# Kernel tuning notes

Hardware: AMD Instinct MI355X
Metric: run time of the kernel (lower is better)

## Reference

```python
import jax, jax.numpy as jnp
import numpy as np

EPS = 1e-5

def _rmsnorm(x, g):
    xf = x.astype(jnp.float32)
    rms = jnp.sqrt(jnp.mean(xf * xf + EPS, axis=-1, keepdims=True))
    return (xf / rms * g).astype(x.dtype)

def setup_inputs() -> dict:
    key = jax.random.key(0)
    ks = jax.random.split(key, 10)
    B, S, D, H, F = 2, 2048, 1024, 16, 4096
    s = 0.02
    return {
        "x": jax.random.normal(ks[0], (B, S, D), jnp.float32),
        "g1": jnp.ones((D,), jnp.float32),
        "wq": jax.random.normal(ks[1], (D, D), jnp.float32) * s,
        "wk": jax.random.normal(ks[2], (D, D), jnp.float32) * s,
        "wv": jax.random.normal(ks[3], (D, D), jnp.float32) * s,
        "wo": jax.random.normal(ks[4], (D, D), jnp.float32) * s,
        "g2": jnp.ones((D,), jnp.float32),
        "w1": jax.random.normal(ks[5], (F, D), jnp.float32) * s,
        "w2": jax.random.normal(ks[6], (D, F), jnp.float32) * s,
        "w3": jax.random.normal(ks[7], (F, D), jnp.float32) * s,
    }

def reference(x, g1, wq, wk, wv, wo, g2, w1, w2, w3):
    B, S, D = x.shape
    H = 16
    hd = D // H
    # --- attention sublayer ---
    xn = _rmsnorm(x, g1)
    q = jnp.einsum('bsd,ed->bse', xn, wq).reshape(B, S, H, hd).transpose(0, 2, 1, 3)
    k = jnp.einsum('bsd,ed->bse', xn, wk).reshape(B, S, H, hd).transpose(0, 2, 1, 3)
    v = jnp.einsum('bsd,ed->bse', xn, wv).reshape(B, S, H, hd).transpose(0, 2, 1, 3)
    scores = jnp.einsum('bhqd,bhkd->bhqk', q, k) / jnp.sqrt(jnp.float32(hd))
    mask = jnp.tril(jnp.ones((S, S), bool))  # causal
    neg = jnp.finfo(scores.dtype).min
    scores = jnp.where(mask[None, None], scores, neg)
    probs = jax.nn.softmax(scores, axis=-1)
    o = jnp.einsum('bhqk,bhkd->bhqd', probs, v)
    o = o.transpose(0, 2, 1, 3).reshape(B, S, D)
    attn_out = jnp.einsum('bsv,dv->bsd', o, wo)
    h = x + attn_out
    # --- SwiGLU sublayer ---
    hn = _rmsnorm(h, g2)
    p1 = jnp.einsum('fd,bsd->bsf', w1, hn)
    p3 = jnp.einsum('fd,bsd->bsf', w3, hn)
    ffn = jnp.einsum('df,bsf->bsd', w2, jax.nn.silu(p1) * p3)
    return h + ffn
```

## Files before the change

kernel.cpp:

```cpp
#include <hip/hip_runtime.h>

typedef __attribute__((ext_vector_type(8))) short short8;
typedef __attribute__((ext_vector_type(4))) float f32x4;

__device__ __forceinline__ unsigned short f2b(float f) {
  union { float f; unsigned u; } v; v.f = f;
  unsigned r = v.u + 0x7fffu + ((v.u >> 16) & 1u);
  return (unsigned short)(r >> 16);
}
__device__ __forceinline__ float b2f(unsigned short b) {
  union { unsigned u; float f; } v; v.u = ((unsigned)b) << 16; return v.f;
}

__device__ __forceinline__ void gload_lds16(const void* g, void* l) {
  __builtin_amdgcn_global_load_lds(
      (const __attribute__((address_space(1))) void*)g,
      (__attribute__((address_space(3))) void*)l, 16, 0, 0);
}

__global__ __launch_bounds__(256) void cvt_k(const float* __restrict__ s,
                                             unsigned short* __restrict__ d, int n4) {
  int i = blockIdx.x * 256 + threadIdx.x;
  if (i >= n4) return;
  float4 v = ((const float4*)s)[i];
  ushort4 o;
  o.x = f2b(v.x); o.y = f2b(v.y); o.z = f2b(v.z); o.w = f2b(v.w);
  ((ushort4*)d)[i] = o;
}

__global__ __launch_bounds__(256) void rmsnorm_k(const float* __restrict__ x,
                                                 const float* __restrict__ g,
                                                 unsigned short* __restrict__ out) {
  const int row = blockIdx.x, tid = threadIdx.x;
  const float4 v = ((const float4*)(x + (size_t)row * 1024))[tid];
  float ss = v.x*v.x + v.y*v.y + v.z*v.z + v.w*v.w;
  #pragma unroll
  for (int d = 32; d > 0; d >>= 1) ss += __shfl_down(ss, d);
  __shared__ float red[4];
  if ((tid & 63) == 0) red[tid >> 6] = ss;
  __syncthreads();
  const float tot = red[0] + red[1] + red[2] + red[3];
  const float sc = rsqrtf(tot * (1.0f/1024.0f) + 1e-5f);
  const float4 gg = ((const float4*)g)[tid];
  ushort4 o;
  o.x = f2b(v.x * sc * gg.x); o.y = f2b(v.y * sc * gg.y);
  o.z = f2b(v.z * sc * gg.z); o.w = f2b(v.w * sc * gg.w);
  ((ushort4*)(out + (size_t)row * 1024))[tid] = o;
}

__global__ __launch_bounds__(256) void gate_k(unsigned short* __restrict__ p13) {
  const size_t i = (size_t)blockIdx.x * 256 + threadIdx.x;
  const int r = (int)(i >> 9);
  const int fc = ((int)i & 511) * 8;
  unsigned short* p1 = p13 + (size_t)r * 8192 + fc;
  const unsigned short* p3 = p13 + (size_t)r * 8192 + 4096 + fc;
  ushort4 a0 = ((const ushort4*)p1)[0], a1 = ((const ushort4*)p1)[1];
  ushort4 b0 = ((const ushort4*)p3)[0], b1 = ((const ushort4*)p3)[1];
  unsigned short va[8] = {a0.x,a0.y,a0.z,a0.w,a1.x,a1.y,a1.z,a1.w};
  unsigned short vb[8] = {b0.x,b0.y,b0.z,b0.w,b1.x,b1.y,b1.z,b1.w};
  unsigned short vo[8];
  #pragma unroll
  for (int j = 0; j < 8; ++j) {
    float f1 = b2f(va[j]), f3 = b2f(vb[j]);
    float s = f1 / (1.0f + __expf(-f1));
    vo[j] = f2b(s * f3);
  }
  ushort4 o0 = {vo[0],vo[1],vo[2],vo[3]}, o1 = {vo[4],vo[5],vo[6],vo[7]};
  ((ushort4*)p1)[0] = o0; ((ushort4*)p1)[1] = o1;
}

template<int EPI>
__global__ __launch_bounds__(256) void gemm_bt(
    const unsigned short* __restrict__ A, const unsigned short* __restrict__ W,
    int N, int K, int lda,
    unsigned short* __restrict__ Cb, const float* __restrict__ res,
    float* __restrict__ Cf, int ldc)
{
  __shared__ unsigned short sA[4096];
  __shared__ unsigned short sB[4096];
  const int tid = threadIdx.x;
  const int w = tid >> 6, l = tid & 63;
  const int l15 = l & 15, l4 = l >> 4;
  const int bm = blockIdx.y * 128, bn = blockIdx.x * 128;
  const int wm = (w >> 1) * 64, wn = (w & 1) * 64;
  const int c0 = w * 128 + l;
  const int ra0 = c0 >> 2,        ka0 = (c0 & 3) * 8;
  const int ra1 = (c0 + 64) >> 2, ka1 = ((c0 + 64) & 3) * 8;
  const unsigned short* Ar0 = A + (size_t)(bm + ra0) * lda + ka0;
  const unsigned short* Ar1 = A + (size_t)(bm + ra1) * lda + ka1;
  const unsigned short* Wr0 = W + (size_t)(bn + ra0) * K + ka0;
  const unsigned short* Wr1 = W + (size_t)(bn + ra1) * K + ka1;
  f32x4 acc[4][4];
  const f32x4 z4 = {0.f, 0.f, 0.f, 0.f};
  #pragma unroll
  for (int i = 0; i < 4; ++i)
    #pragma unroll
    for (int j = 0; j < 4; ++j) acc[i][j] = z4;

  for (int kt = 0; kt < K; kt += 32) {
    gload_lds16(Ar0 + kt, &sA[w * 1024]);
    gload_lds16(Ar1 + kt, &sA[w * 1024 + 512]);
    gload_lds16(Wr0 + kt, &sB[w * 1024]);
    gload_lds16(Wr1 + kt, &sB[w * 1024 + 512]);
    __syncthreads();
    short8 af[4], bf[4];
    #pragma unroll
    for (int mi = 0; mi < 4; ++mi)
      af[mi] = *(const short8*)&sA[(wm + mi*16 + l15)*32 + l4*8];
    #pragma unroll
    for (int ni = 0; ni < 4; ++ni)
      bf[ni] = *(const short8*)&sB[(wn + ni*16 + l15)*32 + l4*8];
    #pragma unroll
    for (int mi = 0; mi < 4; ++mi)
      #pragma unroll
      for (int ni = 0; ni < 4; ++ni)
        acc[mi][ni] = __builtin_amdgcn_mfma_f32_16x16x32_bf16(af[mi], bf[ni], acc[mi][ni], 0, 0, 0);
    __syncthreads();
  }
  #pragma unroll
  for (int mi = 0; mi < 4; ++mi)
    #pragma unroll
    for (int ni = 0; ni < 4; ++ni) {
      const int row0 = bm + wm + mi*16 + l4*4;
      const int col  = bn + wn + ni*16 + l15;
      #pragma unroll
      for (int r = 0; r < 4; ++r) {
        const float v = acc[mi][ni][r];
        if (EPI == 0) {
          Cb[(size_t)(row0 + r) * ldc + col] = f2b(v);
        } else {
          const size_t o = (size_t)(row0 + r) * ldc + col;
          Cf[o] = res[o] + v;
        }
      }
    }
}

__global__ __launch_bounds__(512, 2) void gemm256_bt(
    const unsigned short* __restrict__ A, const unsigned short* __restrict__ W,
    int K, int lda, unsigned short* __restrict__ Cb, int ldc, int nbx)
{
  __shared__ unsigned short sA[4][8192];
  __shared__ unsigned short sB[4][8192];
  const int tid = threadIdx.x;
  const int w = tid >> 6, l = tid & 63;
  const int l15 = l & 15, l4 = l >> 4;
  const int nwg = nbx * gridDim.y;
  const int flat = blockIdx.y * nbx + blockIdx.x;
  const int q8 = nwg >> 3;
  const int sw = (flat & 7) * q8 + (flat >> 3);
  const int bm = (sw / nbx) * 256, bn = (sw % nbx) * 256;

  int rowl[2], coll[2];
  #pragma unroll
  for (int i = 0; i < 2; ++i) {
    const int g = w * 128 + i * 64 + l;
    const int s = g >> 6, j = g & 63;
    const int r = j >> 2, c8 = (j & 3) * 8;
    rowl[i] = s * 16 + r;
    coll[i] = c8 ^ ((r & 8) << 1);
  }
  const unsigned short* As0 = A + (size_t)(bm + rowl[0]) * lda + coll[0];
  const unsigned short* As1 = A + (size_t)(bm + rowl[1]) * lda + coll[1];
  const unsigned short* Ws0 = W + (size_t)(bn + rowl[0]) * K + coll[0];
  const unsigned short* Ws1 = W + (size_t)(bn + rowl[1]) * K + coll[1];
  const int d0 = w * 1024, d1 = w * 1024 + 512;

  const int swzr = (l4 * 8) ^ ((l15 & 8) << 1);
  const int aoff = (w >> 2) * 4096 + l15 * 32 + swzr;
  const int boff = (w & 3) * 2048 + l15 * 32 + swzr;

  f32x4 acc[8][4];
  const f32x4 z4 = {0.f, 0.f, 0.f, 0.f};
  #pragma unroll
  for (int i = 0; i < 8; ++i)
    #pragma unroll
    for (int j = 0; j < 4; ++j) acc[i][j] = z4;

  const int NT = K >> 5;
  #pragma unroll
  for (int p = 0; p < 3; ++p) {
    const int ko = p * 32;
    gload_lds16(As0 + ko, &sA[p][d0]);
    gload_lds16(As1 + ko, &sA[p][d1]);
    gload_lds16(Ws0 + ko, &sB[p][d0]);
    gload_lds16(Ws1 + ko, &sB[p][d1]);
  }
  asm volatile("s_waitcnt vmcnt(8)" ::: "memory");
  __builtin_amdgcn_s_barrier();

  for (int t = 0; t < NT; ++t) {
    const unsigned short* a_ = sA[t & 3];
    const unsigned short* b_ = sB[t & 3];
    const bool st = (t + 3 < NT);
    const int nb = (t + 3) & 3;
    const int ko = (t + 3) * 32;
    short8 bfr[4], afr[4];
    #pragma unroll
    for (int ni = 0; ni < 4; ++ni) bfr[ni] = *(const short8*)&b_[boff + ni * 512];
    #pragma unroll
    for (int mi = 0; mi < 4; ++mi) afr[mi] = *(const short8*)&a_[aoff + mi * 512];
    if (st) { gload_lds16(As0 + ko, &sA[nb][d0]); gload_lds16(Ws0 + ko, &sB[nb][d0]); }
    __builtin_amdgcn_s_barrier();
    asm volatile("s_waitcnt lgkmcnt(0)" ::: "memory");
    __builtin_amdgcn_sched_barrier(0);
    __builtin_amdgcn_s_setprio(1);
    #pragma unroll
    for (int mi = 0; mi < 4; ++mi)
      #pragma unroll
      for (int ni = 0; ni < 4; ++ni)
        acc[mi][ni] = __builtin_amdgcn_mfma_f32_16x16x32_bf16(bfr[ni], afr[mi], acc[mi][ni], 0, 0, 0);
    __builtin_amdgcn_s_setprio(0);
    __builtin_amdgcn_s_barrier();
    #pragma unroll
    for (int mi = 0; mi < 4; ++mi) afr[mi] = *(const short8*)&a_[aoff + (mi + 4) * 512];
    if (st) { gload_lds16(As1 + ko, &sA[nb][d1]); gload_lds16(Ws1 + ko, &sB[nb][d1]); }
    __builtin_amdgcn_s_barrier();
    asm volatile("s_waitcnt lgkmcnt(0)" ::: "memory");
    __builtin_amdgcn_sched_barrier(0);
    __builtin_amdgcn_s_setprio(1);
    #pragma unroll
    for (int mi = 0; mi < 4; ++mi)
      #pragma unroll
      for (int ni = 0; ni < 4; ++ni)
        acc[mi + 4][ni] = __builtin_amdgcn_mfma_f32_16x16x32_bf16(bfr[ni], afr[mi], acc[mi + 4][ni], 0, 0, 0);
    __builtin_amdgcn_s_setprio(0);
    if (t < NT - 3)       asm volatile("s_waitcnt vmcnt(8)" ::: "memory");
    else if (t == NT - 3) asm volatile("s_waitcnt vmcnt(4)" ::: "memory");
    else                  asm volatile("s_waitcnt vmcnt(0)" ::: "memory");
    __builtin_amdgcn_s_barrier();
  }
  #pragma unroll
  for (int mi = 0; mi < 8; ++mi) {
    const int row = bm + (w >> 2) * 128 + mi * 16 + l15;
    #pragma unroll
    for (int ni = 0; ni < 4; ++ni) {
      const int col = bn + (w & 3) * 64 + ni * 16 + l4 * 4;
      ushort4 o = { f2b(acc[mi][ni][0]), f2b(acc[mi][ni][1]),
                    f2b(acc[mi][ni][2]), f2b(acc[mi][ni][3]) };
      *(ushort4*)&Cb[(size_t)row * ldc + col] = o;
    }
  }
}

__global__ __launch_bounds__(256) void vtrans_k(const unsigned short* __restrict__ QKV,
                                                unsigned short* __restrict__ VT) {
  __shared__ unsigned short sT[4096];
  const int st = blockIdx.x, dt = blockIdx.y, b = blockIdx.z;
  const int tid = threadIdx.x;
  #pragma unroll
  for (int half = 0; half < 2; ++half) {
    const int c = tid + half * 256;
    const int r = c >> 3;
    const int ch = c & 7;
    const unsigned short* src =
        QKV + (size_t)(b*2048 + st*64 + r) * 3072 + 2048 + dt*64 + ch*8;
    short8 v = *(const short8*)src;
    *(short8*)&sT[r*64 + ((ch ^ ((r >> 3) & 7)) * 8)] = v;
  }
  __syncthreads();
  #pragma unroll
  for (int half = 0; half < 2; ++half) {
    const int c = tid + half * 256;
    const int od = c >> 3;
    const int oc = c & 7;
    unsigned short tmp[8];
    #pragma unroll
    for (int j = 0; j < 8; ++j) {
      const int srow = oc*8 + j;
      const int chunk = (od >> 3) ^ ((srow >> 3) & 7);
      tmp[j] = sT[srow*64 + chunk*8 + (od & 7)];
    }
    *(short8*)&VT[(size_t)(b*1024 + dt*64 + od) * 2048 + st*64 + oc*8] = *(short8*)tmp;
  }
}

__global__ __launch_bounds__(256) void attn_k(const unsigned short* __restrict__ QKV,
                                              const unsigned short* __restrict__ VT,
                                              unsigned short* __restrict__ Ob)
{
  const int LDQ = 3072;
  const float C2 = 0.125f * 1.44269504088896f;
  const int b = blockIdx.y >> 4, h = blockIdx.y & 15;
  const int tid = threadIdx.x;
  const int w = tid >> 6, l = tid & 63;
  const int l15 = l & 15, l4 = l >> 4;
  const unsigned short* Qg  = QKV + (size_t)(b * 2048) * LDQ + h * 64;
  const unsigned short* Kg  = Qg + 1024;
  const unsigned short* VTg = VT + (size_t)(b * 1024 + h * 64) * 2048;

  __shared__ unsigned short sK[2][4096];
  __shared__ unsigned short sVT[2][4096];
  __shared__ unsigned short sP[4][1152];

  const int rc0 = tid >> 3;
  const int ch0 = (tid & 7) ^ (rc0 & 7);
  const int rc1 = rc0 + 32;
  const unsigned short* Ks0 = Kg  + (size_t)rc0 * LDQ  + ch0 * 8;
  const unsigned short* Ks1 = Kg  + (size_t)rc1 * LDQ  + ch0 * 8;
  const unsigned short* Vs0 = VTg + (size_t)rc0 * 2048 + ch0 * 8;
  const unsigned short* Vs1 = VTg + (size_t)rc1 * 2048 + ch0 * 8;
  const int wun0 = w * 512;
  const int wun1 = 2048 + w * 512;
  const f32x4 z4 = {0.f,0.f,0.f,0.f};

#define ASTAGE(buf, t) do { \
    const size_t ko = (size_t)(t) * 64 * LDQ; const int vo = (t) * 64; \
    gload_lds16(Ks0 + ko, &sK[buf][wun0]); \
    gload_lds16(Ks1 + ko, &sK[buf][wun1]); \
    gload_lds16(Vs0 + vo, &sVT[buf][wun0]); \
    gload_lds16(Vs1 + vo, &sVT[buf][wun1]); } while (0)

  #pragma unroll
  for (int qp = 0; qp < 2; ++qp) {
    const int qtile = (qp == 0) ? (31 - (int)blockIdx.x) : (int)blockIdx.x;
    const int qb = qtile * 64;
    const int qw = qb + w * 16;
    short8 qf[2];
    #pragma unroll
    for (int hc = 0; hc < 2; ++hc)
      qf[hc] = *(const short8*)&Qg[(size_t)(qw + l15) * LDQ + hc*32 + l4*8];

    f32x4 accO[4];
    #pragma unroll
    for (int dt = 0; dt < 4; ++dt) accO[dt] = z4;
    float m_run = -1e30f, l_run = 0.f;

    const int ntB = qtile + 1;
    ASTAGE(0, 0);
    __syncthreads();
    int cur = 0;
    for (int t = 0; t < ntB; ++t) {
      if (t + 1 < ntB) ASTAGE(cur ^ 1, t + 1);
      const int kv = t * 64;
      const unsigned short* Kb = sK[cur];
      const unsigned short* Vb = sVT[cur];
      const int lim = qw + 15 - kv;
      f32x4 sAcc[4];
      #pragma unroll
      for (int nt = 0; nt < 4; ++nt) sAcc[nt] = z4;
      __builtin_amdgcn_s_setprio(1);
      #pragma unroll
      for (int nt = 0; nt < 4; ++nt) {
        if (nt * 16 <= lim) {
          const int krow = nt*16 + l15;
          const short8 kf0 = *(const short8*)&Kb[krow*64 + ((l4 ^ (krow & 7)) * 8)];
          const short8 kf1 = *(const short8*)&Kb[krow*64 + (((4 + l4) ^ (krow & 7)) * 8)];
          sAcc[nt] = __builtin_amdgcn_mfma_f32_16x16x32_bf16(kf0, qf[0], sAcc[nt], 0,0,0);
          sAcc[nt] = __builtin_amdgcn_mfma_f32_16x16x32_bf16(kf1, qf[1], sAcc[nt], 0,0,0);
        }
      }
      __builtin_amdgcn_s_setprio(0);
      const bool bound = (kv + 63 > qw);
      float p[16];
      float mx = -1e30f;
      #pragma unroll
      for (int nt = 0; nt < 4; ++nt)
        #pragma unroll
        for (int r = 0; r < 4; ++r) {
          float s = (nt * 16 <= lim) ? sAcc[nt][r] * C2 : -1e30f;
          if (bound && (kv + nt*16 + l4*4 + r > qw + l15)) s = -1e30f;
          p[nt*4 + r] = s;
          mx = fmaxf(mx, s);
        }
      mx = fmaxf(mx, __shfl_xor(mx, 16));
      mx = fmaxf(mx, __shfl_xor(mx, 32));
      const bool resc = mx > m_run + 8.0f;
      const float mn = resc ? mx : m_run;
      const float f = resc ? exp2f(m_run - mn) : 1.0f;
      m_run = mn;
      float rs = 0.f;
      #pragma unroll
      for (int j = 0; j < 16; ++j) { p[j] = exp2f(p[j] - mn); rs += p[j]; }
      rs += __shfl_xor(rs, 16);
      rs += __shfl_xor(rs, 32);
      l_run = l_run * f + rs;
      if (__any(resc)) {
        float fr[4];
        #pragma unroll
        for (int r = 0; r < 4; ++r) fr[r] = __shfl(f, (l & 48) + l4*4 + r);
        #pragma unroll
        for (int dt = 0; dt < 4; ++dt)
          #pragma unroll
          for (int r = 0; r < 4; ++r) accO[dt][r] *= fr[r];
      }
      #pragma unroll
      for (int nt = 0; nt < 4; ++nt) {
        ushort4 pk = { f2b(p[nt*4]), f2b(p[nt*4+1]), f2b(p[nt*4+2]), f2b(p[nt*4+3]) };
        *(ushort4*)&sP[w][l15*72 + nt*16 + l4*4] = pk;
      }
      short8 pf[2];
      #pragma unroll
      for (int kc = 0; kc < 2; ++kc)
        pf[kc] = *(const short8*)&sP[w][l15*72 + kc*32 + l4*8];
      __builtin_amdgcn_s_setprio(1);
      #pragma unroll
      for (int dt = 0; dt < 4; ++dt) {
        const int vrow = dt*16 + l15;
        const short8 vf0 = *(const short8*)&Vb[vrow*64 + ((l4 ^ (vrow & 7)) * 8)];
        const short8 vf1 = *(const short8*)&Vb[vrow*64 + (((4 + l4) ^ (vrow & 7)) * 8)];
        accO[dt] = __builtin_amdgcn_mfma_f32_16x16x32_bf16(pf[0], vf0, accO[dt], 0,0,0);
        accO[dt] = __builtin_amdgcn_mfma_f32_16x16x32_bf16(pf[1], vf1, accO[dt], 0,0,0);
      }
      __builtin_amdgcn_s_setprio(0);
      __syncthreads();
      cur ^= 1;
    }
    float lr[4];
    #pragma unroll
    for (int r = 0; r < 4; ++r) lr[r] = __shfl(l_run, (l & 48) + l4*4 + r);
    #pragma unroll
    for (int dt = 0; dt < 4; ++dt)
      #pragma unroll
      for (int r = 0; r < 4; ++r) {
        const int row = qw + l4*4 + r;
        Ob[(size_t)(b*2048 + row) * 1024 + h*64 + dt*16 + l15] = f2b(accO[dt][r] / lr[r]);
      }
  }
#undef ASTAGE
}

extern "C" void kernel_launch(void* const* d_in, const int* in_sizes, int n_in,
                              void* d_out, int out_size, void* d_ws, size_t ws_size,
                              hipStream_t stream) {
  const float* x  = (const float*)d_in[0];
  const float* g1 = (const float*)d_in[1];
  const float* wq = (const float*)d_in[2];
  const float* wk = (const float*)d_in[3];
  const float* wv = (const float*)d_in[4];
  const float* wo = (const float*)d_in[5];
  const float* g2 = (const float*)d_in[6];
  const float* w1 = (const float*)d_in[7];
  const float* w2 = (const float*)d_in[8];
  const float* w3 = (const float*)d_in[9];
  float* out = (float*)d_out;
  char* ws = (char*)d_ws;
  (void)in_sizes; (void)n_in; (void)out_size; (void)ws_size;

  unsigned short* Wqkv = (unsigned short*)(ws + 0);
  unsigned short* Wo   = (unsigned short*)(ws + 6291456);
  unsigned short* W13  = (unsigned short*)(ws + 8388608);
  unsigned short* W2   = (unsigned short*)(ws + 25165824);
  unsigned short* XN   = (unsigned short*)(ws + 33554432);
  unsigned short* QKV  = (unsigned short*)(ws + 41943040);
  unsigned short* OB   = (unsigned short*)(ws + 67108864);
  unsigned short* VTb  = (unsigned short*)(ws + 75497472);
  unsigned short* P13  = (unsigned short*)(ws + 41943040);
  float*          H    = (float*)(ws + 109051904);

  cvt_k<<<1024, 256, 0, stream>>>(wq, Wqkv,             262144);
  cvt_k<<<1024, 256, 0, stream>>>(wk, Wqkv + 1048576,   262144);
  cvt_k<<<1024, 256, 0, stream>>>(wv, Wqkv + 2097152,   262144);
  cvt_k<<<1024, 256, 0, stream>>>(wo, Wo,               262144);
  cvt_k<<<4096, 256, 0, stream>>>(w1, W13,             1048576);
  cvt_k<<<4096, 256, 0, stream>>>(w3, W13 + 4194304,   1048576);
  cvt_k<<<4096, 256, 0, stream>>>(w2, W2,              1048576);

  rmsnorm_k<<<4096, 256, 0, stream>>>(x, g1, XN);
  gemm256_bt<<<dim3(12, 16), 512, 0, stream>>>(XN, Wqkv, 1024, 1024, QKV, 3072, 12);
  vtrans_k<<<dim3(32, 16, 2), 256, 0, stream>>>(QKV, VTb);
  attn_k<<<dim3(16, 32), 256, 0, stream>>>(QKV, VTb, OB);
  gemm_bt<1><<<dim3(8, 32), 256, 0, stream>>>(OB, Wo, 1024, 1024, 1024,
                                              nullptr, x, H, 1024);
  rmsnorm_k<<<4096, 256, 0, stream>>>(H, g2, XN);
  gemm256_bt<<<dim3(32, 16), 512, 0, stream>>>(XN, W13, 1024, 1024, P13, 8192, 32);
  gate_k<<<8192, 256, 0, stream>>>(P13);
  gemm_bt<1><<<dim3(8, 32), 256, 0, stream>>>(P13, W2, 1024, 4096, 8192,
                                              nullptr, H, out, 1024);
}
```

Measured before the change: 496.8 us.

## Pipeline 128x128 GEMM with 4-stage LDS ring, swizzle, and vectorized epilogue

Replaces the single-buffered 128-tile GEMM with a 4-buffer LDS ring that prefetches three K-tiles ahead using explicit vmcnt waits and a single barrier per iteration. It also adds an XOR swizzle against LDS bank conflicts, grouped workgroup ordering for L2 reuse, and swapped MFMA operands so the epilogue can write contiguous vectorized bf16/float4 stores. The QKV projection moves from the 256-tile kernel to this 128-tile kernel to get more workgroups. The costs are higher LDS use per block and the risk that the hand-written waitcnt schedule is fragile.

```diff
diff --git a/kernel.cpp b/kernel.cpp
--- a/kernel.cpp
+++ b/kernel.cpp
@@ -70,26 +70,42 @@
 }
 
 template<int EPI>
-__global__ __launch_bounds__(256) void gemm_bt(
+__global__ __launch_bounds__(256, 2) void gemm128p(
     const unsigned short* __restrict__ A, const unsigned short* __restrict__ W,
-    int N, int K, int lda,
-    unsigned short* __restrict__ Cb, const float* __restrict__ res,
-    float* __restrict__ Cf, int ldc)
+    int K, int lda, unsigned short* __restrict__ Cb, const float* __restrict__ res,
+    float* __restrict__ Cf, int ldc, int nbx)
 {
-  __shared__ unsigned short sA[4096];
-  __shared__ unsigned short sB[4096];
+  __shared__ unsigned short sA[4][4096];
+  __shared__ unsigned short sB[4][4096];
   const int tid = threadIdx.x;
   const int w = tid >> 6, l = tid & 63;
   const int l15 = l & 15, l4 = l >> 4;
-  const int bm = blockIdx.y * 128, bn = blockIdx.x * 128;
+  const int nwg = nbx * gridDim.y;
+  const int flat = blockIdx.y * nbx + blockIdx.x;
+  const int q8 = nwg >> 3;
+  const int sw = (flat & 7) * q8 + (flat >> 3);
+  const int bm = (sw / nbx) * 128, bn = (sw % nbx) * 128;
   const int wm = (w >> 1) * 64, wn = (w & 1) * 64;
-  const int c0 = w * 128 + l;
-  const int ra0 = c0 >> 2,        ka0 = (c0 & 3) * 8;
-  const int ra1 = (c0 + 64) >> 2, ka1 = ((c0 + 64) & 3) * 8;
-  const unsigned short* Ar0 = A + (size_t)(bm + ra0) * lda + ka0;
-  const unsigned short* Ar1 = A + (size_t)(bm + ra1) * lda + ka1;
-  const unsigned short* Wr0 = W + (size_t)(bn + ra0) * K + ka0;
-  const unsigned short* Wr1 = W + (size_t)(bn + ra1) * K + ka1;
+
+  int rowl[2], coll[2];
+  #pragma unroll
+  for (int i = 0; i < 2; ++i) {
+    const int g = i * 256 + w * 64 + l;
+    const int s = g >> 6, j = g & 63;
+    const int r = j >> 2, c8 = (j & 3) * 8;
+    rowl[i] = s * 16 + r;
+    coll[i] = c8 ^ ((r & 8) << 1);
+  }
+  const unsigned short* As0 = A + (size_t)(bm + rowl[0]) * lda + coll[0];
+  const unsigned short* As1 = A + (size_t)(bm + rowl[1]) * lda + coll[1];
+  const unsigned short* Ws0 = W + (size_t)(bn + rowl[0]) * K + coll[0];
+  const unsigned short* Ws1 = W + (size_t)(bn + rowl[1]) * K + coll[1];
+  const int d0 = w * 512, d1 = 2048 + w * 512;
+
+  const int swzr = (l4 * 8) ^ ((l15 & 8) << 1);
+  const int aoff = (w >> 1) * 2048 + l15 * 32 + swzr;
+  const int boff = (w & 1) * 2048 + l15 * 32 + swzr;
+
   f32x4 acc[4][4];
   const f32x4 z4 = {0.f, 0.f, 0.f, 0.f};
   #pragma unroll
@@ -97,43 +113,67 @@
     #pragma unroll
     for (int j = 0; j < 4; ++j) acc[i][j] = z4;
 
-  for (int kt = 0; kt < K; kt += 32) {
-    gload_lds16(Ar0 + kt, &sA[w * 1024]);
-    gload_lds16(Ar1 + kt, &sA[w * 1024 + 512]);
-    gload_lds16(Wr0 + kt, &sB[w * 1024]);
-    gload_lds16(Wr1 + kt, &sB[w * 1024 + 512]);
-    __syncthreads();
-    short8 af[4], bf[4];
+  const int NT = K >> 5;
+  #pragma unroll
+  for (int p = 0; p < 3; ++p) {
+    const size_t ko = (size_t)p * 32;
+    gload_lds16(As0 + ko, &sA[p][d0]);
+    gload_lds16(As1 + ko, &sA[p][d1]);
+    gload_lds16(Ws0 + ko, &sB[p][d0]);
+    gload_lds16(Ws1 + ko, &sB[p][d1]);
+  }
+  asm volatile("s_waitcnt vmcnt(8)" ::: "memory");
+  __builtin_amdgcn_s_barrier();
+
+  for (int t = 0; t < NT; ++t) {
+    const unsigned short* a_ = sA[t & 3];
+    const unsigned short* b_ = sB[t & 3];
+    if (t + 3 < NT) {
+      const int nb = (t + 3) & 3;
+      const size_t ko = (size_t)(t + 3) * 32;
+      gload_lds16(As0 + ko, &sA[nb][d0]);
+      gload_lds16(As1 + ko, &sA[nb][d1]);
+      gload_lds16(Ws0 + ko, &sB[nb][d0]);
+      gload_lds16(Ws1 + ko, &sB[nb][d1]);
+    }
+    short8 afr[4], bfr[4];
+    #pragma unroll
+    for (int ni = 0; ni < 4; ++ni) bfr[ni] = *(const short8*)&b_[boff + ni * 512];
+    #pragma unroll
+    for (int mi = 0; mi < 4; ++mi) afr[mi] = *(const short8*)&a_[aoff + mi * 512];
+    asm volatile("s_waitcnt lgkmcnt(0)" ::: "memory");
+    __builtin_amdgcn_sched_barrier(0);
+    __builtin_amdgcn_s_setprio(1);
     #pragma unroll
     for (int mi = 0; mi < 4; ++mi)
-      af[mi] = *(const short8*)&sA[(wm + mi*16 + l15)*32 + l4*8];
-    #pragma unroll
-    for (int ni = 0; ni < 4; ++ni)
-      bf[ni] = *(const short8*)&sB[(wn + ni*16 + l15)*32 + l4*8];
-    #pragma unroll
-    for (int mi = 0; mi < 4; ++mi)
       #pragma unroll
       for (int ni = 0; ni < 4; ++ni)
-        acc[mi][ni] = __builtin_amdgcn_mfma_f32_16x16x32_bf16(af[mi], bf[ni], acc[mi][ni], 0, 0, 0);
-    __syncthreads();
-  }
-  #pragma unroll
-  for (int mi = 0; mi < 4; ++mi)
+        acc[mi][ni] = __builtin_amdgcn_mfma_f32_16x16x32_bf16(bfr[ni], afr[mi], acc[mi][ni], 0, 0, 0);
+    __builtin_amdgcn_s_setprio(0);
+    if (t < NT - 3)       asm volatile("s_waitcnt vmcnt(8)" ::: "memory");
+    else if (t == NT - 3) asm volatile("s_waitcnt vmcnt(4)" ::: "memory");
+    else                  asm volatile("s_waitcnt vmcnt(0)" ::: "memory");
+    __builtin_amdgcn_s_barrier();
+  }
+  #pragma unroll
+  for (int mi = 0; mi < 4; ++mi) {
+    const int row = bm + wm + mi * 16 + l15;
     #pragma unroll
     for (int ni = 0; ni < 4; ++ni) {
-      const int row0 = bm + wm + mi*16 + l4*4;
-      const int col  = bn + wn + ni*16 + l15;
-      #pragma unroll
-      for (int r = 0; r < 4; ++r) {
-        const float v = acc[mi][ni][r];
-        if (EPI == 0) {
-          Cb[(size_t)(row0 + r) * ldc + col] = f2b(v);
-        } else {
-          const size_t o = (size_t)(row0 + r) * ldc + col;
-          Cf[o] = res[o] + v;
-        }
+      const int col = bn + wn + ni * 16 + l4 * 4;
+      if (EPI == 0) {
+        ushort4 o = { f2b(acc[mi][ni][0]), f2b(acc[mi][ni][1]),
+                      f2b(acc[mi][ni][2]), f2b(acc[mi][ni][3]) };
+        *(ushort4*)&Cb[(size_t)row * ldc + col] = o;
+      } else {
+        const size_t o = (size_t)row * ldc + col;
+        const float4 rv = *(const float4*)&res[o];
+        float4 ov = { rv.x + acc[mi][ni][0], rv.y + acc[mi][ni][1],
+                      rv.z + acc[mi][ni][2], rv.w + acc[mi][ni][3] };
+        *(float4*)&Cf[o] = ov;
       }
     }
+  }
 }
 
 __global__ __launch_bounds__(512, 2) void gemm256_bt(
@@ -457,14 +497,15 @@
   cvt_k<<<4096, 256, 0, stream>>>(w2, W2,              1048576);
 
   rmsnorm_k<<<4096, 256, 0, stream>>>(x, g1, XN);
-  gemm256_bt<<<dim3(12, 16), 512, 0, stream>>>(XN, Wqkv, 1024, 1024, QKV, 3072, 12);
+  gemm128p<0><<<dim3(24, 32), 256, 0, stream>>>(XN, Wqkv, 1024, 1024,
+                                                QKV, nullptr, nullptr, 3072, 24);
   vtrans_k<<<dim3(32, 16, 2), 256, 0, stream>>>(QKV, VTb);
   attn_k<<<dim3(16, 32), 256, 0, stream>>>(QKV, VTb, OB);
-  gemm_bt<1><<<dim3(8, 32), 256, 0, stream>>>(OB, Wo, 1024, 1024, 1024,
-                                              nullptr, x, H, 1024);
+  gemm128p<1><<<dim3(8, 32), 256, 0, stream>>>(OB, Wo, 1024, 1024,
+                                               nullptr, x, H, 1024, 8);
   rmsnorm_k<<<4096, 256, 0, stream>>>(H, g2, XN);
   gemm256_bt<<<dim3(32, 16), 512, 0, stream>>>(XN, W13, 1024, 1024, P13, 8192, 32);
   gate_k<<<8192, 256, 0, stream>>>(P13);
-  gemm_bt<1><<<dim3(8, 32), 256, 0, stream>>>(P13, W2, 1024, 4096, 8192,
-                                              nullptr, H, out, 1024);
-}
+  gemm128p<1><<<dim3(8, 32), 256, 0, stream>>>(P13, W2, 4096, 8192,
+                                               nullptr, H, out, 1024, 8);
+}
```

Result: faster. 481.1 us (-3.2%).
